# Kernel optimization log

Measured on AMD Instinct MI355X. Metric: run time of the kernel, lower is better.

The kernel has to match this reference:

```python
import jax, jax.numpy as jnp
import numpy as np

EPS = 1e-5  # torch BatchNorm1d default

def _bn(z, g, b):
    # training-mode BatchNorm1d: per-feature batch mean, biased variance
    m = jnp.mean(z, axis=0)
    v = jnp.mean((z - m) ** 2, axis=0)
    return (z - m) * jax.lax.rsqrt(v + EPS) * g + b

def _cell(x, h, c, Wx, Wh, gx, bx, gh, bh):
    gates = _bn(x @ Wx.T, gx, bx) + _bn(h @ Wh.T, gh, bh)  # [B, 4H]
    f, i, o, g = jnp.split(gates, 4, axis=1)  # chunk order f,i,o,g
    c2 = jax.nn.sigmoid(f) * c + jax.nn.sigmoid(i) * jnp.tanh(g)
    h2 = jax.nn.sigmoid(o) * jnp.tanh(c2)
    return h2, c2

def setup_inputs() -> dict:
    key = jax.random.key(0)
    B, H, OUT = 16384, 512, 256
    IN0 = 257  # input_size - 1 (x_dim 256 + y_dim 1)
    ks = jax.random.split(key, 16)
    def lin(k, fo, fi):
        s = 1.0 / np.sqrt(fi)
        return jax.random.uniform(k, (fo, fi), jnp.float32, -s, s)
    return {
        "x": jax.random.normal(ks[0], (B, 256), jnp.float32),
        "y": jax.random.normal(ks[1], (B, 1), jnp.float32),
        "h0": jax.random.normal(ks[2], (2, B, H), jnp.float32),
        "c0": jax.random.normal(ks[3], (2, B, H), jnp.float32),
        "Wx0": lin(ks[4], 4 * H, IN0),
        "Wh0": lin(ks[5], 4 * H, H),
        "gx0": jnp.ones((4 * H,), jnp.float32),
        "bx0": jnp.zeros((4 * H,), jnp.float32),
        "gh0": jnp.ones((4 * H,), jnp.float32),
        "bh0": jnp.zeros((4 * H,), jnp.float32),
        "Wx1": lin(ks[6], 4 * H, H),
        "Wh1": lin(ks[7], 4 * H, H),
        "gx1": jnp.ones((4 * H,), jnp.float32),
        "bx1": jnp.zeros((4 * H,), jnp.float32),
        "gh1": jnp.ones((4 * H,), jnp.float32),
        "bh1": jnp.zeros((4 * H,), jnp.float32),
        "Wo": lin(ks[8], OUT, H),
        "bo": jnp.zeros((OUT,), jnp.float32),
    }

def reference(x, y, h0, c0, Wx0, Wh0, gx0, bx0, gh0, bh0,
              Wx1, Wh1, gx1, bx1, gh1, bh1, Wo, bo):
    inp = jnp.concatenate([x, y], axis=1)  # [B, 257]
    h1, c1 = _cell(inp, h0[0], c0[0], Wx0, Wh0, gx0, bx0, gh0, bh0)
    h2, c2 = _cell(h1, h0[1], c0[1], Wx1, Wh1, gx1, bx1, gh1, bh1)
    out = h2 @ Wo.T + bo  # [B, output_size]
    return (out, jnp.stack([h1, h2]), jnp.stack([c1, c2]))
```

## Files before the change

kernel.cpp:

```cpp
#include <hip/hip_runtime.h>
#include <cstdint>

typedef unsigned short u16;
typedef unsigned int u32;
typedef float floatx4 __attribute__((ext_vector_type(4)));
typedef __bf16 bf16x8 __attribute__((ext_vector_type(8)));
typedef u16 u16x4 __attribute__((ext_vector_type(4)));

__device__ __forceinline__ u16 f2b(float f) {
  u32 u = __builtin_bit_cast(u32, f);
  u32 r = (u + 0x7fffu + ((u >> 16) & 1u)) >> 16;
  return (u16)r;
}
__device__ __forceinline__ float b2f(u16 b) {
  return __builtin_bit_cast(float, (u32)b << 16);
}
__device__ __forceinline__ float sigf(float x) { return 1.f / (1.f + __expf(-x)); }
__device__ __forceinline__ float tanhfast(float x) { return 2.f / (1.f + __expf(-2.f * x)) - 1.f; }

#define GLDS(gp, lp) __builtin_amdgcn_global_load_lds( \
    (const __attribute__((address_space(1))) u32*)(gp), \
    (__attribute__((address_space(3))) u32*)(lp), 16, 0, 0)

template <int STATS, int BIAS>
__global__ __launch_bounds__(256) void gemm_bt(
    const u16* __restrict__ A, const u16* __restrict__ W, void* __restrict__ Cv,
    int N, int K, float* __restrict__ ssum, float* __restrict__ ssq,
    const float* __restrict__ bias) {
  __shared__ u16 As[128 * 32];
  __shared__ u16 Bs[128 * 32];
  const int tid = threadIdx.x;
  const int lane = tid & 63;
  const int wave = tid >> 6;
  const int wm = (wave >> 1) << 6;
  const int wn = (wave & 1) << 6;
  const int m0 = blockIdx.y * 128;
  const int n0 = blockIdx.x * 128;
  const u16* Ab = A + (size_t)m0 * K;
  const u16* Wb = W + (size_t)n0 * K;
  const size_t soff = (size_t)(tid >> 2) * K + ((tid & 3) << 3);
  const size_t soff2 = soff + (size_t)64 * K;
  const int fr = lane & 15;
  const int fq = lane >> 4;
  const int aoff = fr * 32 + fq * 8;

  floatx4 acc[4][4] = {};

  for (int k0 = 0; k0 < K; k0 += 32) {
    __syncthreads();
    GLDS(Ab + soff + k0, &As[tid * 8]);
    GLDS(Ab + soff2 + k0, &As[tid * 8 + 2048]);
    GLDS(Wb + soff + k0, &Bs[tid * 8]);
    GLDS(Wb + soff2 + k0, &Bs[tid * 8 + 2048]);
    __syncthreads();
    bf16x8 af[4], bfv[4];
#pragma unroll
    for (int i = 0; i < 4; ++i) af[i] = *(const bf16x8*)&As[(wm + i * 16) * 32 + aoff];
#pragma unroll
    for (int j = 0; j < 4; ++j) bfv[j] = *(const bf16x8*)&Bs[(wn + j * 16) * 32 + aoff];
#pragma unroll
    for (int i = 0; i < 4; ++i)
#pragma unroll
      for (int j = 0; j < 4; ++j)
        acc[i][j] = __builtin_amdgcn_mfma_f32_16x16x32_bf16(af[i], bfv[j], acc[i][j], 0, 0, 0);
  }

  if (BIAS) {
    float* C = (float*)Cv;
#pragma unroll
    for (int i = 0; i < 4; ++i)
#pragma unroll
      for (int j = 0; j < 4; ++j) {
        const int col = n0 + wn + j * 16 + fr;
        const float bv = bias[col];
#pragma unroll
        for (int r = 0; r < 4; ++r) {
          const int row = m0 + wm + i * 16 + fq * 4 + r;
          C[(size_t)row * N + col] = acc[i][j][r] + bv;
        }
      }
  } else {
    u16* C = (u16*)Cv;
#pragma unroll
    for (int i = 0; i < 4; ++i)
#pragma unroll
      for (int j = 0; j < 4; ++j) {
        const int col = n0 + wn + j * 16 + fr;
#pragma unroll
        for (int r = 0; r < 4; ++r) {
          const int row = m0 + wm + i * 16 + fq * 4 + r;
          C[(size_t)row * N + col] = f2b(acc[i][j][r]);
        }
      }
  }

  if (STATS) {
#pragma unroll
    for (int j = 0; j < 4; ++j) {
      float s = 0.f, q = 0.f;
#pragma unroll
      for (int i = 0; i < 4; ++i)
#pragma unroll
        for (int r = 0; r < 4; ++r) {
          const float v = acc[i][j][r];
          s += v;
          q += v * v;
        }
      s += __shfl_xor(s, 16);
      s += __shfl_xor(s, 32);
      q += __shfl_xor(q, 16);
      q += __shfl_xor(q, 32);
      if (fq == 0) {
        atomicAdd(&ssum[n0 + wn + j * 16 + fr], s);
        atomicAdd(&ssq[n0 + wn + j * 16 + fr], q);
      }
    }
  }
}

__global__ void pad_inp_k(const float* __restrict__ x, const float* __restrict__ y,
                          u16* __restrict__ o) {
  const int idx = blockIdx.x * 256 + threadIdx.x;
  const int b = idx / 288;
  const int c = idx - b * 288;
  float v = 0.f;
  if (c < 256) v = x[b * 256 + c];
  else if (c == 256) v = y[b];
  o[idx] = f2b(v);
}

__global__ void pad_w_k(const float* __restrict__ w, u16* __restrict__ o) {
  const int idx = blockIdx.x * 256 + threadIdx.x;
  const int r = idx / 288;
  const int c = idx - r * 288;
  o[idx] = f2b(c < 257 ? w[r * 257 + c] : 0.f);
}

__global__ void f2b_k(const float4* __restrict__ in, u16x4* __restrict__ o, int n4) {
  const int idx = blockIdx.x * 256 + threadIdx.x;
  if (idx < n4) {
    const float4 v = in[idx];
    u16x4 r;
    r.x = f2b(v.x);
    r.y = f2b(v.y);
    r.z = f2b(v.z);
    r.w = f2b(v.w);
    o[idx] = r;
  }
}

__global__ void coef_k(const float* __restrict__ st, const float* __restrict__ gx,
                       const float* __restrict__ bx, const float* __restrict__ gh,
                       const float* __restrict__ bh, float* __restrict__ cf, float invB) {
  const int j = blockIdx.x * 256 + threadIdx.x;
  const float mx = st[j] * invB;
  const float vx = st[2048 + j] * invB - mx * mx;
  const float ax = gx[j] * rsqrtf(vx + 1e-5f);
  const float mh = st[4096 + j] * invB;
  const float vh = st[6144 + j] * invB - mh * mh;
  const float ah = gh[j] * rsqrtf(vh + 1e-5f);
  cf[j] = ax;
  cf[2048 + j] = ah;
  cf[4096 + j] = bx[j] - mx * ax + bh[j] - mh * ah;
}

__global__ void cell_k(const u16* __restrict__ Zx, const u16* __restrict__ Zh,
                       const float* __restrict__ coef, const float* __restrict__ cin,
                       float* __restrict__ hout, float* __restrict__ cout,
                       u16* __restrict__ hb) {
  const int idx = blockIdx.x * 256 + threadIdx.x;
  const int b = idx >> 8;
  const int j2 = (idx & 255) << 1;
  const size_t rb = (size_t)b << 11;
  float gv[4][2];
#pragma unroll
  for (int g = 0; g < 4; ++g) {
    const int col = (g << 9) + j2;
    const u32 zx = *(const u32*)(Zx + rb + col);
    const u32 zh = *(const u32*)(Zh + rb + col);
#pragma unroll
    for (int t = 0; t < 2; ++t) {
      const float zxv = b2f((u16)(zx >> (16 * t)));
      const float zhv = b2f((u16)(zh >> (16 * t)));
      gv[g][t] = coef[col + t] * zxv + coef[2048 + col + t] * zhv + coef[4096 + col + t];
    }
  }
  const size_t ob = ((size_t)b << 9) + j2;
  const float2 cp = *(const float2*)(cin + ob);
  float cn[2], hn[2];
#pragma unroll
  for (int t = 0; t < 2; ++t) {
    const float cprev = t ? cp.y : cp.x;
    const float cc = sigf(gv[0][t]) * cprev + sigf(gv[1][t]) * tanhfast(gv[3][t]);
    cn[t] = cc;
    hn[t] = sigf(gv[2][t]) * tanhfast(cc);
  }
  *(float2*)(cout + ob) = make_float2(cn[0], cn[1]);
  *(float2*)(hout + ob) = make_float2(hn[0], hn[1]);
  *(u32*)(hb + ob) = (u32)f2b(hn[0]) | ((u32)f2b(hn[1]) << 16);
}

extern "C" void kernel_launch(void* const* d_in, const int* in_sizes, int n_in,
                              void* d_out, int out_size, void* d_ws, size_t ws_size,
                              hipStream_t stream) {
  (void)in_sizes; (void)n_in; (void)out_size; (void)ws_size;
  constexpr int B = 16384, H = 512, G = 2048, KP = 288, K1 = 512, NOUT = 256;

  const float* x = (const float*)d_in[0];
  const float* y = (const float*)d_in[1];
  const float* h0 = (const float*)d_in[2];
  const float* c0 = (const float*)d_in[3];
  const float* Wx0 = (const float*)d_in[4];
  const float* Wh0 = (const float*)d_in[5];
  const float* gx0 = (const float*)d_in[6];
  const float* bx0 = (const float*)d_in[7];
  const float* gh0 = (const float*)d_in[8];
  const float* bh0 = (const float*)d_in[9];
  const float* Wx1 = (const float*)d_in[10];
  const float* Wh1 = (const float*)d_in[11];
  const float* gx1 = (const float*)d_in[12];
  const float* bx1 = (const float*)d_in[13];
  const float* gh1 = (const float*)d_in[14];
  const float* bh1 = (const float*)d_in[15];
  const float* Wo = (const float*)d_in[16];
  const float* bo = (const float*)d_in[17];

  char* p = (char*)d_ws;
  u16* Zx = (u16*)p;   p += (size_t)B * G * 2;
  u16* Zh = (u16*)p;   p += (size_t)B * G * 2;
  u16* h0b = (u16*)p;  p += (size_t)2 * B * H * 2;
  u16* h1b = (u16*)p;  p += (size_t)B * H * 2;
  u16* inpb = (u16*)p; p += (size_t)B * KP * 2;
  u16* wx0b = (u16*)p; p += (size_t)G * KP * 2;
  u16* wh0b = (u16*)p; p += (size_t)G * K1 * 2;
  u16* wx1b = (u16*)p; p += (size_t)G * K1 * 2;
  u16* wh1b = (u16*)p; p += (size_t)G * K1 * 2;
  u16* wob = (u16*)p;  p += (size_t)NOUT * K1 * 2;
  float* stats = (float*)p; p += (size_t)8 * G * 4;
  float* coef = (float*)p;  p += (size_t)6 * G * 4;

  float* out_o = (float*)d_out;
  float* h_o = out_o + (size_t)B * NOUT;
  float* c_o = h_o + (size_t)2 * B * H;

  hipMemsetAsync(stats, 0, (size_t)8 * G * sizeof(float), stream);

  pad_inp_k<<<B * KP / 256, 256, 0, stream>>>(x, y, inpb);
  pad_w_k<<<G * KP / 256, 256, 0, stream>>>(Wx0, wx0b);
  f2b_k<<<2 * B * H / 4 / 256, 256, 0, stream>>>((const float4*)h0, (u16x4*)h0b, 2 * B * H / 4);
  f2b_k<<<G * K1 / 4 / 256, 256, 0, stream>>>((const float4*)Wh0, (u16x4*)wh0b, G * K1 / 4);
  f2b_k<<<G * K1 / 4 / 256, 256, 0, stream>>>((const float4*)Wx1, (u16x4*)wx1b, G * K1 / 4);
  f2b_k<<<G * K1 / 4 / 256, 256, 0, stream>>>((const float4*)Wh1, (u16x4*)wh1b, G * K1 / 4);
  f2b_k<<<NOUT * K1 / 4 / 256, 256, 0, stream>>>((const float4*)Wo, (u16x4*)wob, NOUT * K1 / 4);

  const dim3 blk(256);
  const dim3 gbig(G / 128, B / 128);

  gemm_bt<1, 0><<<gbig, blk, 0, stream>>>(inpb, wx0b, Zx, G, KP, stats + 0 * G, stats + 1 * G, nullptr);
  gemm_bt<1, 0><<<gbig, blk, 0, stream>>>(h0b, wh0b, Zh, G, K1, stats + 2 * G, stats + 3 * G, nullptr);
  coef_k<<<G / 256, 256, 0, stream>>>(stats, gx0, bx0, gh0, bh0, coef, 1.f / B);
  cell_k<<<B, 256, 0, stream>>>(Zx, Zh, coef, c0, h_o, c_o, h1b);

  gemm_bt<1, 0><<<gbig, blk, 0, stream>>>(h1b, wx1b, Zx, G, K1, stats + 4 * G, stats + 5 * G, nullptr);
  gemm_bt<1, 0><<<gbig, blk, 0, stream>>>(h0b + (size_t)B * H, wh1b, Zh, G, K1, stats + 6 * G, stats + 7 * G, nullptr);
  coef_k<<<G / 256, 256, 0, stream>>>(stats + 4 * G, gx1, bx1, gh1, bh1, coef + 3 * G, 1.f / B);
  cell_k<<<B, 256, 0, stream>>>(Zx, Zh, coef + 3 * G, c0 + (size_t)B * H,
                                h_o + (size_t)B * H, c_o + (size_t)B * H, h1b);

  const dim3 gout(NOUT / 128, B / 128);
  gemm_bt<0, 1><<<gout, blk, 0, stream>>>(h1b, wob, out_o, NOUT, K1, nullptr, nullptr, bo);
}
```

Before: 652.3 us.

## Merge paired GEMMs into dual launch, batch conversions, vectorize epilogue stores

Swaps the MFMA operand order so each lane holds four consecutive columns, which allows packed 4-element bf16 and float4 stores instead of scattered scalar stores. The BN statistics reduction is reworked to match the new layout. The x-path and h-path GEMMs of each cell are launched as one grid with z=2, which fills more of the GPU in a single launch. The seven conversion kernels plus the memset are merged into two kernels to cut launch overhead. The risk is that the transposed accumulator layout needs correct indexing everywhere it is used.

```diff
diff --git a/kernel.cpp b/kernel.cpp
--- a/kernel.cpp
+++ b/kernel.cpp
@@ -22,11 +22,106 @@
     (const __attribute__((address_space(1))) u32*)(gp), \
     (__attribute__((address_space(3))) u32*)(lp), 16, 0, 0)
 
-template <int STATS, int BIAS>
-__global__ __launch_bounds__(256) void gemm_bt(
-    const u16* __restrict__ A, const u16* __restrict__ W, void* __restrict__ Cv,
-    int N, int K, float* __restrict__ ssum, float* __restrict__ ssq,
-    const float* __restrict__ bias) {
+struct GemmArgs {
+  const u16* A;
+  const u16* W;
+  u16* C;
+  int K;
+  float* ssum;
+  float* ssq;
+};
+
+__device__ __forceinline__ void gemm_body(const GemmArgs g, int N,
+                                          u16* As, u16* Bs) {
+  const int tid = threadIdx.x;
+  const int lane = tid & 63;
+  const int wave = tid >> 6;
+  const int wm = (wave >> 1) << 6;
+  const int wn = (wave & 1) << 6;
+  const int m0 = blockIdx.y * 128;
+  const int n0 = blockIdx.x * 128;
+  const int K = g.K;
+  const u16* Ab = g.A + (size_t)m0 * K;
+  const u16* Wb = g.W + (size_t)n0 * K;
+  const size_t soff = (size_t)(tid >> 2) * K + ((tid & 3) << 3);
+  const size_t soff2 = soff + (size_t)64 * K;
+  const int fr = lane & 15;
+  const int fq = lane >> 4;
+  const int aoff = fr * 32 + fq * 8;
+
+  floatx4 acc[4][4] = {};
+
+  for (int k0 = 0; k0 < K; k0 += 32) {
+    __syncthreads();
+    GLDS(Ab + soff + k0, &As[tid * 8]);
+    GLDS(Ab + soff2 + k0, &As[tid * 8 + 2048]);
+    GLDS(Wb + soff + k0, &Bs[tid * 8]);
+    GLDS(Wb + soff2 + k0, &Bs[tid * 8 + 2048]);
+    __syncthreads();
+    bf16x8 af[4], bfv[4];
+#pragma unroll
+    for (int i = 0; i < 4; ++i) af[i] = *(const bf16x8*)&As[(wm + i * 16) * 32 + aoff];
+#pragma unroll
+    for (int j = 0; j < 4; ++j) bfv[j] = *(const bf16x8*)&Bs[(wn + j * 16) * 32 + aoff];
+#pragma unroll
+    for (int i = 0; i < 4; ++i)
+#pragma unroll
+      for (int j = 0; j < 4; ++j)
+        acc[i][j] = __builtin_amdgcn_mfma_f32_16x16x32_bf16(bfv[j], af[i], acc[i][j], 0, 0, 0);
+  }
+
+  u16* C = g.C;
+#pragma unroll
+  for (int i = 0; i < 4; ++i) {
+    const size_t row = (size_t)(m0 + wm + i * 16 + fr);
+#pragma unroll
+    for (int j = 0; j < 4; ++j) {
+      const int cb = n0 + wn + j * 16 + fq * 4;
+      u16x4 pk;
+#pragma unroll
+      for (int r = 0; r < 4; ++r) pk[r] = f2b(acc[i][j][r]);
+      *(u16x4*)&C[row * N + cb] = pk;
+    }
+  }
+
+#pragma unroll
+  for (int j = 0; j < 4; ++j) {
+    const int cb = n0 + wn + j * 16 + fq * 4;
+    floatx4 s = {}, q = {};
+#pragma unroll
+    for (int i = 0; i < 4; ++i)
+#pragma unroll
+      for (int r = 0; r < 4; ++r) {
+        const float v = acc[i][j][r];
+        s[r] += v;
+        q[r] += v * v;
+      }
+#pragma unroll
+    for (int st = 1; st <= 8; st <<= 1)
+#pragma unroll
+      for (int r = 0; r < 4; ++r) {
+        s[r] += __shfl_xor(s[r], st);
+        q[r] += __shfl_xor(q[r], st);
+      }
+    if (fr == 0) {
+#pragma unroll
+      for (int r = 0; r < 4; ++r) {
+        atomicAdd(&g.ssum[cb + r], s[r]);
+        atomicAdd(&g.ssq[cb + r], q[r]);
+      }
+    }
+  }
+}
+
+__global__ __launch_bounds__(256) void gemm_dual(GemmArgs g0, GemmArgs g1, int N) {
+  __shared__ u16 As[128 * 32];
+  __shared__ u16 Bs[128 * 32];
+  gemm_body(blockIdx.z ? g1 : g0, N, As, Bs);
+}
+
+__global__ __launch_bounds__(256) void gemm_bias(
+    const u16* __restrict__ A, const u16* __restrict__ W, float* __restrict__ C,
+    int N, int K, const float* __restrict__ bias) {
   __shared__ u16 As[128 * 32];
   __shared__ u16 Bs[128 * 32];
   const int tid = threadIdx.x;
@@ -45,7 +140,6 @@
   const int aoff = fr * 32 + fq * 8;
 
   floatx4 acc[4][4] = {};
-
   for (int k0 = 0; k0 < K; k0 += 32) {
     __syncthreads();
     GLDS(Ab + soff + k0, &As[tid * 8]);
@@ -62,91 +156,74 @@
     for (int i = 0; i < 4; ++i)
 #pragma unroll
       for (int j = 0; j < 4; ++j)
-        acc[i][j] = __builtin_amdgcn_mfma_f32_16x16x32_bf16(af[i], bfv[j], acc[i][j], 0, 0, 0);
-  }
-
-  if (BIAS) {
-    float* C = (float*)Cv;
-#pragma unroll
-    for (int i = 0; i < 4; ++i)
-#pragma unroll
-      for (int j = 0; j < 4; ++j) {
-        const int col = n0 + wn + j * 16 + fr;
-        const float bv = bias[col];
-#pragma unroll
-        for (int r = 0; r < 4; ++r) {
-          const int row = m0 + wm + i * 16 + fq * 4 + r;
-          C[(size_t)row * N + col] = acc[i][j][r] + bv;
-        }
-      }
+        acc[i][j] = __builtin_amdgcn_mfma_f32_16x16x32_bf16(bfv[j], af[i], acc[i][j], 0, 0, 0);
+  }
+#pragma unroll
+  for (int i = 0; i < 4; ++i) {
+    const size_t row = (size_t)(m0 + wm + i * 16 + fr);
+#pragma unroll
+    for (int j = 0; j < 4; ++j) {
+      const int cb = n0 + wn + j * 16 + fq * 4;
+      const floatx4 bv = *(const floatx4*)&bias[cb];
+      floatx4 o;
+#pragma unroll
+      for (int r = 0; r < 4; ++r) o[r] = acc[i][j][r] + bv[r];
+      *(floatx4*)&C[row * N + cb] = o;
+    }
+  }
+}
+
+__global__ void conv_in_k(const float* __restrict__ x, const float* __restrict__ y,
+                          u16* __restrict__ inpb, const float4* __restrict__ h04,
+                          u16x4* __restrict__ h0b4, float* __restrict__ stats) {
+  const int blk = blockIdx.x;
+  const int tid = threadIdx.x;
+  if (blk < 18432) {
+    const int idx = blk * 256 + tid;
+    const int b = idx / 288;
+    const int c = idx - b * 288;
+    float v = 0.f;
+    if (c < 256) v = x[b * 256 + c];
+    else if (c == 256) v = y[b];
+    inpb[idx] = f2b(v);
+  } else if (blk < 18432 + 16384) {
+    const int id = (blk - 18432) * 256 + tid;
+    const float4 v = h04[id];
+    u16x4 r;
+    r.x = f2b(v.x); r.y = f2b(v.y); r.z = f2b(v.z); r.w = f2b(v.w);
+    h0b4[id] = r;
   } else {
-    u16* C = (u16*)Cv;
-#pragma unroll
-    for (int i = 0; i < 4; ++i)
-#pragma unroll
-      for (int j = 0; j < 4; ++j) {
-        const int col = n0 + wn + j * 16 + fr;
-#pragma unroll
-        for (int r = 0; r < 4; ++r) {
-          const int row = m0 + wm + i * 16 + fq * 4 + r;
-          C[(size_t)row * N + col] = f2b(acc[i][j][r]);
-        }
-      }
-  }
-
-  if (STATS) {
-#pragma unroll
-    for (int j = 0; j < 4; ++j) {
-      float s = 0.f, q = 0.f;
-#pragma unroll
-      for (int i = 0; i < 4; ++i)
-#pragma unroll
-        for (int r = 0; r < 4; ++r) {
-          const float v = acc[i][j][r];
-          s += v;
-          q += v * v;
-        }
-      s += __shfl_xor(s, 16);
-      s += __shfl_xor(s, 32);
-      q += __shfl_xor(q, 16);
-      q += __shfl_xor(q, 32);
-      if (fq == 0) {
-        atomicAdd(&ssum[n0 + wn + j * 16 + fr], s);
-        atomicAdd(&ssq[n0 + wn + j * 16 + fr], q);
-      }
-    }
-  }
-}
-
-__global__ void pad_inp_k(const float* __restrict__ x, const float* __restrict__ y,
-                          u16* __restrict__ o) {
-  const int idx = blockIdx.x * 256 + threadIdx.x;
-  const int b = idx / 288;
-  const int c = idx - b * 288;
-  float v = 0.f;
-  if (c < 256) v = x[b * 256 + c];
-  else if (c == 256) v = y[b];
-  o[idx] = f2b(v);
-}
-
-__global__ void pad_w_k(const float* __restrict__ w, u16* __restrict__ o) {
-  const int idx = blockIdx.x * 256 + threadIdx.x;
-  const int r = idx / 288;
-  const int c = idx - r * 288;
-  o[idx] = f2b(c < 257 ? w[r * 257 + c] : 0.f);
-}
-
-__global__ void f2b_k(const float4* __restrict__ in, u16x4* __restrict__ o, int n4) {
-  const int idx = blockIdx.x * 256 + threadIdx.x;
-  if (idx < n4) {
-    const float4 v = in[idx];
-    u16x4 r;
-    r.x = f2b(v.x);
-    r.y = f2b(v.y);
-    r.z = f2b(v.z);
-    r.w = f2b(v.w);
-    o[idx] = r;
-  }
+    const int id = (blk - 18432 - 16384) * 256 + tid;
+    stats[id] = 0.f;
+  }
+}
+
+__global__ void conv_w_k(const float* __restrict__ Wx0, u16* __restrict__ wx0b,
+                         const float4* __restrict__ Wh0, u16x4* __restrict__ wh0b,
+                         const float4* __restrict__ Wx1, u16x4* __restrict__ wx1b,
+                         const float4* __restrict__ Wh1, u16x4* __restrict__ wh1b,
+                         const float4* __restrict__ Wo, u16x4* __restrict__ wob) {
+  const int blk = blockIdx.x;
+  const int tid = threadIdx.x;
+  if (blk < 2304) {
+    const int idx = blk * 256 + tid;
+    const int r = idx / 288;
+    const int c = idx - r * 288;
+    wx0b[idx] = f2b(c < 257 ? Wx0[r * 257 + c] : 0.f);
+    return;
+  }
+  const float4* src;
+  u16x4* dst;
+  int rel = blk - 2304;
+  if (rel < 1024) { src = Wh0; dst = wh0b; }
+  else if (rel < 2048) { src = Wx1; dst = wx1b; rel -= 1024; }
+  else if (rel < 3072) { src = Wh1; dst = wh1b; rel -= 2048; }
+  else { src = Wo; dst = wob; rel -= 3072; }
+  const int id = rel * 256 + tid;
+  const float4 v = src[id];
+  u16x4 r;
+  r.x = f2b(v.x); r.y = f2b(v.y); r.z = f2b(v.z); r.w = f2b(v.w);
+  dst[id] = r;
 }
 
 __global__ void coef_k(const float* __restrict__ st, const float* __restrict__ gx,
@@ -243,30 +320,33 @@
   float* h_o = out_o + (size_t)B * NOUT;
   float* c_o = h_o + (size_t)2 * B * H;
 
-  hipMemsetAsync(stats, 0, (size_t)8 * G * sizeof(float), stream);
-
-  pad_inp_k<<<B * KP / 256, 256, 0, stream>>>(x, y, inpb);
-  pad_w_k<<<G * KP / 256, 256, 0, stream>>>(Wx0, wx0b);
-  f2b_k<<<2 * B * H / 4 / 256, 256, 0, stream>>>((const float4*)h0, (u16x4*)h0b, 2 * B * H / 4);
-  f2b_k<<<G * K1 / 4 / 256, 256, 0, stream>>>((const float4*)Wh0, (u16x4*)wh0b, G * K1 / 4);
-  f2b_k<<<G * K1 / 4 / 256, 256, 0, stream>>>((const float4*)Wx1, (u16x4*)wx1b, G * K1 / 4);
-  f2b_k<<<G * K1 / 4 / 256, 256, 0, stream>>>((const float4*)Wh1, (u16x4*)wh1b, G * K1 / 4);
-  f2b_k<<<NOUT * K1 / 4 / 256, 256, 0, stream>>>((const float4*)Wo, (u16x4*)wob, NOUT * K1 / 4);
+  conv_in_k<<<18432 + 16384 + 64, 256, 0, stream>>>(x, y, inpb, (const float4*)h0,
+                                                    (u16x4*)h0b, stats);
+  conv_w_k<<<2304 + 3200, 256, 0, stream>>>(Wx0, wx0b, (const float4*)Wh0, (u16x4*)wh0b,
+                                            (const float4*)Wx1, (u16x4*)wx1b,
+                                            (const float4*)Wh1, (u16x4*)wh1b,
+                                            (const float4*)Wo, (u16x4*)wob);
 
   const dim3 blk(256);
-  const dim3 gbig(G / 128, B / 128);
-
-  gemm_bt<1, 0><<<gbig, blk, 0, stream>>>(inpb, wx0b, Zx, G, KP, stats + 0 * G, stats + 1 * G, nullptr);
-  gemm_bt<1, 0><<<gbig, blk, 0, stream>>>(h0b, wh0b, Zh, G, K1, stats + 2 * G, stats + 3 * G, nullptr);
+  const dim3 gdual(G / 128, B / 128, 2);
+
+  {
+    GemmArgs ga{inpb, wx0b, Zx, KP, stats + 0 * G, stats + 1 * G};
+    GemmArgs gb{h0b, wh0b, Zh, K1, stats + 2 * G, stats + 3 * G};
+    gemm_dual<<<gdual, blk, 0, stream>>>(ga, gb, G);
+  }
   coef_k<<<G / 256, 256, 0, stream>>>(stats, gx0, bx0, gh0, bh0, coef, 1.f / B);
   cell_k<<<B, 256, 0, stream>>>(Zx, Zh, coef, c0, h_o, c_o, h1b);
 
-  gemm_bt<1, 0><<<gbig, blk, 0, stream>>>(h1b, wx1b, Zx, G, K1, stats + 4 * G, stats + 5 * G, nullptr);
-  gemm_bt<1, 0><<<gbig, blk, 0, stream>>>(h0b + (size_t)B * H, wh1b, Zh, G, K1, stats + 6 * G, stats + 7 * G, nullptr);
+  {
+    GemmArgs ga{h1b, wx1b, Zx, K1, stats + 4 * G, stats + 5 * G};
+    GemmArgs gb{h0b + (size_t)B * H, wh1b, Zh, K1, stats + 6 * G, stats + 7 * G};
+    gemm_dual<<<gdual, blk, 0, stream>>>(ga, gb, G);
+  }
   coef_k<<<G / 256, 256, 0, stream>>>(stats + 4 * G, gx1, bx1, gh1, bh1, coef + 3 * G, 1.f / B);
   cell_k<<<B, 256, 0, stream>>>(Zx, Zh, coef + 3 * G, c0 + (size_t)B * H,
                                 h_o + (size_t)B * H, c_o + (size_t)B * H, h1b);
 
-  const dim3 gout(NOUT / 128, B / 128);
-  gemm_bt<0, 1><<<gout, blk, 0, stream>>>(h1b, wob, out_o, NOUT, K1, nullptr, nullptr, bo);
-}
+  const dim3 gout(NOUT / 128, B / 128, 1);
+  gemm_bias<<<gout, blk, 0, stream>>>(h1b, wob, out_o, NOUT, K1, bo);
+}
```

After: 678.4 us. 4.0% more time.
